# Kernel tuning notes

Measured on AMD Instinct MI355X. Metric: run time of the kernel, lower is better.

The kernel has to match this reference:

```python
import jax, jax.numpy as jnp
import numpy as np


def setup_inputs() -> dict:
    key = jax.random.key(0)
    k1, k2, k3 = jax.random.split(key, 3)
    B, Lq, Lk, D = 8, 512, 512, 64
    q = jax.random.normal(k1, (B, Lq, D), dtype=jnp.float32)
    k = jax.random.normal(k2, (B, Lk, D), dtype=jnp.float32)
    v = jax.random.normal(k3, (B, Lk, D), dtype=jnp.float32)
    return {"q": q, "k": k, "v": v}


def reference(q, k, v):
    scale = 1.0
    # broadcast add: [B, Lq, 1, D] + [B, 1, Lk, D] -> [B, Lq, Lk, D]
    scores = jnp.sum(scale * jnp.tanh(q[:, :, None, :] + k[:, None, :, :]), axis=-1)  # [B, Lq, Lk]
    attn = jax.nn.softmax(scores, axis=-1)
    out = jnp.einsum('bqk,bkd->bqd', attn, v)
    return out
```

## Files before the change

### kernel.cpp

```cpp
#include <hip/hip_runtime.h>

namespace {
constexpr int Bn = 8, LQ = 512, LK = 512, Dn = 64;
constexpr int T = 512, QT = 8, KT = 64, NT = LK / KT;
constexpr float C2 = 2.8853900817779268f;

__device__ __forceinline__ void gload_lds16(const float* g, float* l) {
  __builtin_amdgcn_global_load_lds(
      (const __attribute__((address_space(1))) void*)g,
      (__attribute__((address_space(3))) void*)l, 16, 0, 0);
}

__global__ __launch_bounds__(T, 4)
void addattn(const float* __restrict__ Q, const float* __restrict__ K,
             const float* __restrict__ V, float* __restrict__ O)
{
  __shared__ __align__(16) float ekL[2][KT][68];
  __shared__ __align__(16) float vL [2][KT][Dn];
  __shared__ __align__(16) float eqs[QT][Dn];
  __shared__ __align__(16) float pL [QT][68];
  __shared__ float lsum[QT];

  const int t    = threadIdx.x;
  const int w    = t >> 6;
  const int lane = t & 63;
  const int ks   = (t >> 4) & 3;
  const int dq   = t & 15;
  const int krow = t >> 3;
  const int kc8  = (t & 7) * 8;
  const int bb   = blockIdx.x >> 6;
  const int q0   = (blockIdx.x & 63) * QT;

  const float* Kt = K + (size_t)bb * LK * Dn;
  const float* Vt = V + (size_t)bb * LK * Dn;

  if (t < 128) {
    const int r = t >> 4, d4 = t & 15;
    float4 qv = *(const float4*)(Q + (size_t)(bb * LQ + q0 + r) * Dn + d4 * 4);
    float4 e;
    e.x = __builtin_amdgcn_exp2f(qv.x * C2);
    e.y = __builtin_amdgcn_exp2f(qv.y * C2);
    e.z = __builtin_amdgcn_exp2f(qv.z * C2);
    e.w = __builtin_amdgcn_exp2f(qv.w * C2);
    *(float4*)&eqs[r][d4 * 4] = e;
  }
  {
    const float* g = Vt + (size_t)(w * 8) * Dn + lane * 4;
    float* l = &vL[0][w * 8][0];
    gload_lds16(g, l);
    gload_lds16(g + 256, l + 256);
  }
  {
    float4 k0v = *(const float4*)(Kt + (size_t)krow * Dn + kc8);
    float4 k1v = *(const float4*)(Kt + (size_t)krow * Dn + kc8 + 4);
    float4 e0, e1;
    e0.x = __builtin_amdgcn_exp2f(k0v.x * C2);
    e0.y = __builtin_amdgcn_exp2f(k0v.y * C2);
    e0.z = __builtin_amdgcn_exp2f(k0v.z * C2);
    e0.w = __builtin_amdgcn_exp2f(k0v.w * C2);
    e1.x = __builtin_amdgcn_exp2f(k1v.x * C2);
    e1.y = __builtin_amdgcn_exp2f(k1v.y * C2);
    e1.z = __builtin_amdgcn_exp2f(k1v.z * C2);
    e1.w = __builtin_amdgcn_exp2f(k1v.w * C2);
    *(float4*)&ekL[0][krow][kc8]     = e0;
    *(float4*)&ekL[0][krow][kc8 + 4] = e1;
  }
  __syncthreads();

  float  dsum = 0.f;
  float4 acc  = make_float4(0.f, 0.f, 0.f, 0.f);
  int buf = 0;

  for (int tile = 0; tile < NT; ++tile) {
    float4 kv0, kv1;
    const bool more = (tile + 1 < NT);
    if (more) {
      const int kb = (tile + 1) * KT;
      const float* g = Vt + (size_t)(kb + w * 8) * Dn + lane * 4;
      float* l = &vL[buf ^ 1][w * 8][0];
      gload_lds16(g, l);
      gload_lds16(g + 256, l + 256);
      kv0 = *(const float4*)(Kt + (size_t)(kb + krow) * Dn + kc8);
      kv1 = *(const float4*)(Kt + (size_t)(kb + krow) * Dn + kc8 + 4);
    }

    {
      float a0 = 0.f, a1 = 0.f, a2 = 0.f, a3 = 0.f;
      const float* ekr = &ekL[buf][lane][0];
      const float* eqr = &eqs[w][0];
      #pragma unroll
      for (int d4 = 0; d4 < 16; ++d4) {
        const float4 e = *(const float4*)(eqr + d4 * 4);
        const float4 x = *(const float4*)(ekr + d4 * 4);
        a0 += __builtin_amdgcn_rcpf(fmaf(e.x, x.x, 1.f));
        a1 += __builtin_amdgcn_rcpf(fmaf(e.y, x.y, 1.f));
        a2 += __builtin_amdgcn_rcpf(fmaf(e.z, x.z, 1.f));
        a3 += __builtin_amdgcn_rcpf(fmaf(e.w, x.w, 1.f));
      }
      const float p = __builtin_amdgcn_exp2f(-C2 * ((a0 + a1) + (a2 + a3)));
      dsum += p;
      pL[w][lane] = p;
    }

    {
      const float* vrow = &vL[buf][ks * 16][dq * 4];
      const float* prow = &pL[w][ks * 16];
      #pragma unroll
      for (int j = 0; j < 16; ++j) {
        const float4 v4 = *(const float4*)(vrow + j * Dn);
        const float  pw = prow[j];
        acc.x = fmaf(pw, v4.x, acc.x);
        acc.y = fmaf(pw, v4.y, acc.y);
        acc.z = fmaf(pw, v4.z, acc.z);
        acc.w = fmaf(pw, v4.w, acc.w);
      }
    }

    if (more) {
      float4 e0, e1;
      e0.x = __builtin_amdgcn_exp2f(kv0.x * C2);
      e0.y = __builtin_amdgcn_exp2f(kv0.y * C2);
      e0.z = __builtin_amdgcn_exp2f(kv0.z * C2);
      e0.w = __builtin_amdgcn_exp2f(kv0.w * C2);
      e1.x = __builtin_amdgcn_exp2f(kv1.x * C2);
      e1.y = __builtin_amdgcn_exp2f(kv1.y * C2);
      e1.z = __builtin_amdgcn_exp2f(kv1.z * C2);
      e1.w = __builtin_amdgcn_exp2f(kv1.w * C2);
      *(float4*)&ekL[buf ^ 1][krow][kc8]     = e0;
      *(float4*)&ekL[buf ^ 1][krow][kc8 + 4] = e1;
    }

    __syncthreads();
    buf ^= 1;
  }

  #pragma unroll
  for (int m = 1; m < 64; m <<= 1) dsum += __shfl_xor(dsum, m);
  if (lane == 0) lsum[w] = dsum;

  float* scr = &ekL[0][0][0];
  *(float4*)(scr + (size_t)(w * 4 + ks) * 64 + dq * 4) = acc;
  __syncthreads();

  if (t < 128) {
    const int r = t >> 4, d4 = t & 15;
    float4 o = make_float4(0.f, 0.f, 0.f, 0.f);
    #pragma unroll
    for (int s = 0; s < 4; ++s) {
      const float4 c = *(const float4*)(scr + (size_t)(r * 4 + s) * 64 + d4 * 4);
      o.x += c.x; o.y += c.y; o.z += c.z; o.w += c.w;
    }
    const float inv = 1.0f / lsum[r];
    o.x *= inv; o.y *= inv; o.z *= inv; o.w *= inv;
    *(float4*)(O + (size_t)(bb * LQ + q0 + r) * Dn + d4 * 4) = o;
  }
}
}

extern "C" void kernel_launch(void* const* d_in, const int* in_sizes, int n_in,
                              void* d_out, int out_size, void* d_ws, size_t ws_size,
                              hipStream_t stream) {
  (void)in_sizes; (void)n_in; (void)d_ws; (void)ws_size; (void)out_size;
  const float* Q = (const float*)d_in[0];
  const float* K = (const float*)d_in[1];
  const float* V = (const float*)d_in[2];
  float* O = (float*)d_out;
  addattn<<<dim3(Bn * (LQ / QT)), dim3(T), 0, stream>>>(Q, K, V, O);
}
```

Baseline: 80.99 us.

## Precompute exp(q),exp(k) in prep kernel and register-tile 4 queries per wave

Adds a prep kernel that computes exp2(2x*log2e) for Q and K once into workspace, storing K with an XOR swizzle so LDS reads avoid bank conflicts without padding. The main kernel loads pre-exponentiated K and V tiles straight into LDS via global_load_lds, raises the tile sizes (16 queries, 128 keys), and gives each wave 4 query rows, so every ek and V value loaded is reused four times in registers. This removes the per-block redundant exp of K and cuts LDS traffic per FLOP. In exchange it adds a second launch, workspace traffic, more registers per thread, and half as many blocks.

Result: slower. 92.48 us (+14.2%).

```diff
diff --git a/kernel.cpp b/kernel.cpp
--- a/kernel.cpp
+++ b/kernel.cpp
@@ -2,157 +2,166 @@
 
 namespace {
 constexpr int Bn = 8, LQ = 512, LK = 512, Dn = 64;
-constexpr int T = 512, QT = 8, KT = 64, NT = LK / KT;
+constexpr int T = 512, QT = 16, KT = 128, NT = LK / KT;
 constexpr float C2 = 2.8853900817779268f;
 
-__device__ __forceinline__ void gload_lds16(const float* g, float* l) {
+
+__device__ __forceinline__ void gl_lds16(const float* g, float* l) {
   __builtin_amdgcn_global_load_lds(
       (const __attribute__((address_space(1))) void*)g,
       (__attribute__((address_space(3))) void*)l, 16, 0, 0);
 }
 
-__global__ __launch_bounds__(T, 4)
-void addattn(const float* __restrict__ Q, const float* __restrict__ K,
+__global__ __launch_bounds__(256)
+void prep(const float* __restrict__ Q, const float* __restrict__ K,
+          float* __restrict__ eqG, float* __restrict__ ekG) {
+  const int g = blockIdx.x * 256 + threadIdx.x;
+  const int row = g >> 6, c = g & 63;
+  eqG[g] = __builtin_amdgcn_exp2f(Q[g] * C2);
+  ekG[row * 64 + (c ^ ((row & 7) * 4))] = __builtin_amdgcn_exp2f(K[g] * C2);
+}
+
+__global__ __launch_bounds__(T, 2)
+void addattn(const float* __restrict__ eqG, const float* __restrict__ ekG,
              const float* __restrict__ V, float* __restrict__ O)
 {
-  __shared__ __align__(16) float ekL[2][KT][68];
+  __shared__ __align__(16) float ekL[2][KT][Dn];
   __shared__ __align__(16) float vL [2][KT][Dn];
-  __shared__ __align__(16) float eqs[QT][Dn];
-  __shared__ __align__(16) float pL [QT][68];
-  __shared__ float lsum[QT];
+  __shared__ __align__(16) float pL [QT][132];
+  __shared__ float scrD[8][4];
 
   const int t    = threadIdx.x;
+  const int bb   = blockIdx.x >> 5;
+  const int q0   = (blockIdx.x & 31) * QT;
   const int w    = t >> 6;
   const int lane = t & 63;
-  const int ks   = (t >> 4) & 3;
-  const int dq   = t & 15;
-  const int krow = t >> 3;
-  const int kc8  = (t & 7) * 8;
-  const int bb   = blockIdx.x >> 6;
-  const int q0   = (blockIdx.x & 63) * QT;
+  const int qhu  = __builtin_amdgcn_readfirstlane(w >> 1);
+  const int khu  = __builtin_amdgcn_readfirstlane(w & 1);
+  const int dq   = lane & 15;
+  const int kg   = lane >> 4;
+  const int sw   = (lane & 7) * 4;
 
-  const float* Kt = K + (size_t)bb * LK * Dn;
-  const float* Vt = V + (size_t)bb * LK * Dn;
+  const float* eqw = eqG + (size_t)(bb * LQ + q0 + qhu * 4) * Dn;
+  const float* ekB = ekG + (size_t)(bb * LK) * Dn;
+  const float* vB  = V   + (size_t)(bb * LK) * Dn;
 
-  if (t < 128) {
-    const int r = t >> 4, d4 = t & 15;
-    float4 qv = *(const float4*)(Q + (size_t)(bb * LQ + q0 + r) * Dn + d4 * 4);
-    float4 e;
-    e.x = __builtin_amdgcn_exp2f(qv.x * C2);
-    e.y = __builtin_amdgcn_exp2f(qv.y * C2);
-    e.z = __builtin_amdgcn_exp2f(qv.z * C2);
-    e.w = __builtin_amdgcn_exp2f(qv.w * C2);
-    *(float4*)&eqs[r][d4 * 4] = e;
-  }
-  {
-    const float* g = Vt + (size_t)(w * 8) * Dn + lane * 4;
-    float* l = &vL[0][w * 8][0];
-    gload_lds16(g, l);
-    gload_lds16(g + 256, l + 256);
-  }
-  {
-    float4 k0v = *(const float4*)(Kt + (size_t)krow * Dn + kc8);
-    float4 k1v = *(const float4*)(Kt + (size_t)krow * Dn + kc8 + 4);
-    float4 e0, e1;
-    e0.x = __builtin_amdgcn_exp2f(k0v.x * C2);
-    e0.y = __builtin_amdgcn_exp2f(k0v.y * C2);
-    e0.z = __builtin_amdgcn_exp2f(k0v.z * C2);
-    e0.w = __builtin_amdgcn_exp2f(k0v.w * C2);
-    e1.x = __builtin_amdgcn_exp2f(k1v.x * C2);
-    e1.y = __builtin_amdgcn_exp2f(k1v.y * C2);
-    e1.z = __builtin_amdgcn_exp2f(k1v.z * C2);
-    e1.w = __builtin_amdgcn_exp2f(k1v.w * C2);
-    *(float4*)&ekL[0][krow][kc8]     = e0;
-    *(float4*)&ekL[0][krow][kc8 + 4] = e1;
-  }
+  auto stage = [&](int buf, int k0) {
+    const float* gs = ekB + (size_t)k0 * Dn;
+    const float* vs = vB  + (size_t)k0 * Dn;
+    float* le = &ekL[buf][0][0];
+    float* lv = &vL [buf][0][0];
+    #pragma unroll
+    for (int r = 0; r < 4; ++r) {
+      gl_lds16(gs + r * 2048 + t * 4, le + r * 2048 + t * 4);
+      gl_lds16(vs + r * 2048 + t * 4, lv + r * 2048 + t * 4);
+    }
+  };
+
+  stage(0, 0);
   __syncthreads();
 
-  float  dsum = 0.f;
-  float4 acc  = make_float4(0.f, 0.f, 0.f, 0.f);
-  int buf = 0;
+  float acc[4][4];
+  #pragma unroll
+  for (int qi = 0; qi < 4; ++qi) {
+    acc[qi][0] = 0.f; acc[qi][1] = 0.f; acc[qi][2] = 0.f; acc[qi][3] = 0.f;
+  }
+  float ds4[4] = {0.f, 0.f, 0.f, 0.f};
 
   for (int tile = 0; tile < NT; ++tile) {
-    float4 kv0, kv1;
-    const bool more = (tile + 1 < NT);
-    if (more) {
-      const int kb = (tile + 1) * KT;
-      const float* g = Vt + (size_t)(kb + w * 8) * Dn + lane * 4;
-      float* l = &vL[buf ^ 1][w * 8][0];
-      gload_lds16(g, l);
-      gload_lds16(g + 256, l + 256);
-      kv0 = *(const float4*)(Kt + (size_t)(kb + krow) * Dn + kc8);
-      kv1 = *(const float4*)(Kt + (size_t)(kb + krow) * Dn + kc8 + 4);
-    }
+    const int buf = tile & 1;
+    if (tile + 1 < NT) stage(buf ^ 1, (tile + 1) * KT);
 
     {
-      float a0 = 0.f, a1 = 0.f, a2 = 0.f, a3 = 0.f;
-      const float* ekr = &ekL[buf][lane][0];
-      const float* eqr = &eqs[w][0];
+      const float* ekrow = &ekL[buf][khu * 64 + lane][0];
+      float a0[4] = {0.f, 0.f, 0.f, 0.f};
+      float a1[4] = {0.f, 0.f, 0.f, 0.f};
       #pragma unroll
       for (int d4 = 0; d4 < 16; ++d4) {
-        const float4 e = *(const float4*)(eqr + d4 * 4);
-        const float4 x = *(const float4*)(ekr + d4 * 4);
-        a0 += __builtin_amdgcn_rcpf(fmaf(e.x, x.x, 1.f));
-        a1 += __builtin_amdgcn_rcpf(fmaf(e.y, x.y, 1.f));
-        a2 += __builtin_amdgcn_rcpf(fmaf(e.z, x.z, 1.f));
-        a3 += __builtin_amdgcn_rcpf(fmaf(e.w, x.w, 1.f));
+        const float4 x  = *(const float4*)(ekrow + ((d4 * 4) ^ sw));
+        const float4 e0 = *(const float4*)(eqw + 0 * Dn + d4 * 4);
+        const float4 e1 = *(const float4*)(eqw + 1 * Dn + d4 * 4);
+        const float4 e2 = *(const float4*)(eqw + 2 * Dn + d4 * 4);
+        const float4 e3 = *(const float4*)(eqw + 3 * Dn + d4 * 4);
+        a0[0] += __builtin_amdgcn_rcpf(fmaf(e0.x, x.x, 1.f));
+        a1[0] += __builtin_amdgcn_rcpf(fmaf(e0.y, x.y, 1.f));
+        a0[0] += __builtin_amdgcn_rcpf(fmaf(e0.z, x.z, 1.f));
+        a1[0] += __builtin_amdgcn_rcpf(fmaf(e0.w, x.w, 1.f));
+        a0[1] += __builtin_amdgcn_rcpf(fmaf(e1.x, x.x, 1.f));
+        a1[1] += __builtin_amdgcn_rcpf(fmaf(e1.y, x.y, 1.f));
+        a0[1] += __builtin_amdgcn_rcpf(fmaf(e1.z, x.z, 1.f));
+        a1[1] += __builtin_amdgcn_rcpf(fmaf(e1.w, x.w, 1.f));
+        a0[2] += __builtin_amdgcn_rcpf(fmaf(e2.x, x.x, 1.f));
+        a1[2] += __builtin_amdgcn_rcpf(fmaf(e2.y, x.y, 1.f));
+        a0[2] += __builtin_amdgcn_rcpf(fmaf(e2.z, x.z, 1.f));
+        a1[2] += __builtin_amdgcn_rcpf(fmaf(e2.w, x.w, 1.f));
+        a0[3] += __builtin_amdgcn_rcpf(fmaf(e3.x, x.x, 1.f));
+        a1[3] += __builtin_amdgcn_rcpf(fmaf(e3.y, x.y, 1.f));
+        a0[3] += __builtin_amdgcn_rcpf(fmaf(e3.z, x.z, 1.f));
+        a1[3] += __builtin_amdgcn_rcpf(fmaf(e3.w, x.w, 1.f));
       }
-      const float p = __builtin_amdgcn_exp2f(-C2 * ((a0 + a1) + (a2 + a3)));
-      dsum += p;
-      pL[w][lane] = p;
-    }
-
-    {
-      const float* vrow = &vL[buf][ks * 16][dq * 4];
-      const float* prow = &pL[w][ks * 16];
       #pragma unroll
-      for (int j = 0; j < 16; ++j) {
-        const float4 v4 = *(const float4*)(vrow + j * Dn);
-        const float  pw = prow[j];
-        acc.x = fmaf(pw, v4.x, acc.x);
-        acc.y = fmaf(pw, v4.y, acc.y);
-        acc.z = fmaf(pw, v4.z, acc.z);
-        acc.w = fmaf(pw, v4.w, acc.w);
+      for (int qi = 0; qi < 4; ++qi) {
+        const float p = __builtin_amdgcn_exp2f(-C2 * (a0[qi] + a1[qi]));
+        ds4[qi] += p;
+        pL[qhu * 4 + qi][khu * 64 + lane] = p;
       }
     }
 
-    if (more) {
-      float4 e0, e1;
-      e0.x = __builtin_amdgcn_exp2f(kv0.x * C2);
-      e0.y = __builtin_amdgcn_exp2f(kv0.y * C2);
-      e0.z = __builtin_amdgcn_exp2f(kv0.z * C2);
-      e0.w = __builtin_amdgcn_exp2f(kv0.w * C2);
-      e1.x = __builtin_amdgcn_exp2f(kv1.x * C2);
-      e1.y = __builtin_amdgcn_exp2f(kv1.y * C2);
-      e1.z = __builtin_amdgcn_exp2f(kv1.z * C2);
-      e1.w = __builtin_amdgcn_exp2f(kv1.w * C2);
-      *(float4*)&ekL[buf ^ 1][krow][kc8]     = e0;
-      *(float4*)&ekL[buf ^ 1][krow][kc8 + 4] = e1;
+    float pcf[4][16];
+    #pragma unroll
+    for (int qi = 0; qi < 4; ++qi)
+      #pragma unroll
+      for (int jq = 0; jq < 4; ++jq)
+        *(float4*)&pcf[qi][jq * 4] =
+            *(const float4*)&pL[qhu * 4 + qi][khu * 64 + kg * 16 + jq * 4];
+
+    {
+      const float* vbase = &vL[buf][khu * 64 + kg * 16][0] + dq * 4;
+      #pragma unroll
+      for (int j = 0; j < 16; ++j) {
+        const float4 v4 = *(const float4*)(vbase + j * Dn);
+        #pragma unroll
+        for (int qi = 0; qi < 4; ++qi) {
+          const float pj = pcf[qi][j];
+          acc[qi][0] = fmaf(pj, v4.x, acc[qi][0]);
+          acc[qi][1] = fmaf(pj, v4.y, acc[qi][1]);
+          acc[qi][2] = fmaf(pj, v4.z, acc[qi][2]);
+          acc[qi][3] = fmaf(pj, v4.w, acc[qi][3]);
+        }
+      }
     }
 
     __syncthreads();
-    buf ^= 1;
   }
 
   #pragma unroll
-  for (int m = 1; m < 64; m <<= 1) dsum += __shfl_xor(dsum, m);
-  if (lane == 0) lsum[w] = dsum;
+  for (int qi = 0; qi < 4; ++qi) {
+    float s = ds4[qi];
+    #pragma unroll
+    for (int m = 1; m < 64; m <<= 1) s += __shfl_xor(s, m);
+    if (lane == 0) scrD[w][qi] = s;
+  }
 
   float* scr = &ekL[0][0][0];
-  *(float4*)(scr + (size_t)(w * 4 + ks) * 64 + dq * 4) = acc;
+  const int slice = khu * 4 + kg;
+  #pragma unroll
+  for (int qi = 0; qi < 4; ++qi)
+    *(float4*)(scr + (size_t)(slice * QT + qhu * 4 + qi) * Dn + dq * 4) =
+        make_float4(acc[qi][0], acc[qi][1], acc[qi][2], acc[qi][3]);
   __syncthreads();
 
-  if (t < 128) {
-    const int r = t >> 4, d4 = t & 15;
+  if (t < 256) {
+    const int r = t >> 4, d4c = t & 15;
     float4 o = make_float4(0.f, 0.f, 0.f, 0.f);
     #pragma unroll
-    for (int s = 0; s < 4; ++s) {
-      const float4 c = *(const float4*)(scr + (size_t)(r * 4 + s) * 64 + d4 * 4);
+    for (int s8 = 0; s8 < 8; ++s8) {
+      const float4 c = *(const float4*)(scr + (size_t)(s8 * QT + r) * Dn + d4c * 4);
       o.x += c.x; o.y += c.y; o.z += c.z; o.w += c.w;
     }
-    const float inv = 1.0f / lsum[r];
+    const int rqh = r >> 2, rqi = r & 3;
+    const float inv = 1.0f / (scrD[rqh * 2 + 0][rqi] + scrD[rqh * 2 + 1][rqi]);
     o.x *= inv; o.y *= inv; o.z *= inv; o.w *= inv;
-    *(float4*)(O + (size_t)(bb * LQ + q0 + r) * Dn + d4 * 4) = o;
+    *(float4*)(O + (size_t)(bb * LQ + q0 + r) * Dn + d4c * 4) = o;
   }
 }
 }
@@ -160,10 +169,13 @@
 extern "C" void kernel_launch(void* const* d_in, const int* in_sizes, int n_in,
                               void* d_out, int out_size, void* d_ws, size_t ws_size,
                               hipStream_t stream) {
-  (void)in_sizes; (void)n_in; (void)d_ws; (void)ws_size; (void)out_size;
+  (void)in_sizes; (void)n_in; (void)out_size; (void)ws_size;
   const float* Q = (const float*)d_in[0];
   const float* K = (const float*)d_in[1];
   const float* V = (const float*)d_in[2];
-  float* O = (float*)d_out;
-  addattn<<<dim3(Bn * (LQ / QT)), dim3(T), 0, stream>>>(Q, K, V, O);
+  float* O   = (float*)d_out;
+  float* eqG = (float*)d_ws;
+  float* ekG = eqG + (size_t)Bn * LQ * Dn;
+  prep<<<dim3(Bn * LK * Dn / 256), dim3(256), 0, stream>>>(Q, K, eqG, ekG);
+  addattn<<<dim3(Bn * (LQ / QT)), dim3(T), 0, stream>>>(eqG, ekG, V, O);
 }
```

## Register-tile exp(q) per wave, split D across lanes with shuffle reduction

Applied to the files above, without the earlier changes.

Each wave now handles two query rows and half of the key tile. Four lanes share one key column and each covers 16 of the D dimensions, reducing partial sums with shuffles. exp(q) values stay in registers instead of shared memory, and each exp(k) LDS load is reused for two queries, which halves LDS traffic in the score loop. The P·V stage and the final reduction are remapped to match. This adds register pressure and extra shuffles.

Result: slower. 83.39 us (+3.0%).

```diff
diff --git a/kernel.cpp b/kernel.cpp
--- a/kernel.cpp
+++ b/kernel.cpp
@@ -5,7 +5,8 @@
 constexpr int T = 512, QT = 8, KT = 64, NT = LK / KT;
 constexpr float C2 = 2.8853900817779268f;
 
-__device__ __forceinline__ void gload_lds16(const float* g, float* l) {
+
+__device__ __forceinline__ void gl_lds16(const float* g, float* l) {
   __builtin_amdgcn_global_load_lds(
       (const __attribute__((address_space(1))) void*)g,
       (__attribute__((address_space(3))) void*)l, 16, 0, 0);
@@ -17,98 +18,151 @@
 {
   __shared__ __align__(16) float ekL[2][KT][68];
   __shared__ __align__(16) float vL [2][KT][Dn];
-  __shared__ __align__(16) float eqs[QT][Dn];
   __shared__ __align__(16) float pL [QT][68];
-  __shared__ float lsum[QT];
+  __shared__ float scrD[2][QT];
 
   const int t    = threadIdx.x;
   const int w    = t >> 6;
   const int lane = t & 63;
-  const int ks   = (t >> 4) & 3;
-  const int dq   = t & 15;
-  const int krow = t >> 3;
-  const int kc8  = (t & 7) * 8;
+  const int qq   = w >> 1;
+  const int kq   = w & 1;
+  const int dsub = lane & 3;
+  const int k16  = lane >> 2;
+  const int pq   = lane >> 5;
+  const int kh   = (lane >> 4) & 1;
+  const int dq   = lane & 15;
+  const int srow = t >> 3;
+  const int scol = (t & 7) * 8;
   const int bb   = blockIdx.x >> 6;
   const int q0   = (blockIdx.x & 63) * QT;
 
   const float* Kt = K + (size_t)bb * LK * Dn;
   const float* Vt = V + (size_t)bb * LK * Dn;
 
-  if (t < 128) {
-    const int r = t >> 4, d4 = t & 15;
-    float4 qv = *(const float4*)(Q + (size_t)(bb * LQ + q0 + r) * Dn + d4 * 4);
-    float4 e;
-    e.x = __builtin_amdgcn_exp2f(qv.x * C2);
-    e.y = __builtin_amdgcn_exp2f(qv.y * C2);
-    e.z = __builtin_amdgcn_exp2f(qv.z * C2);
-    e.w = __builtin_amdgcn_exp2f(qv.w * C2);
-    *(float4*)&eqs[r][d4 * 4] = e;
-  }
+  auto stageV = [&](int buf, int k0) {
+    const float* vs = Vt + (size_t)k0 * Dn;
+    float* lv = &vL[buf][0][0];
+    gl_lds16(vs + t * 4,        lv + t * 4);
+    gl_lds16(vs + 2048 + t * 4, lv + 2048 + t * 4);
+  };
+
+  float4 eqr[8];
+  #pragma unroll
+  for (int q = 0; q < 2; ++q) {
+    #pragma unroll
+    for (int j = 0; j < 4; ++j) {
+      float4 v = *(const float4*)(Q + (size_t)(bb * LQ + q0 + qq * 2 + q) * Dn
+                                  + dsub * 16 + j * 4);
+      v.x = __builtin_amdgcn_exp2f(v.x * C2);
+      v.y = __builtin_amdgcn_exp2f(v.y * C2);
+      v.z = __builtin_amdgcn_exp2f(v.z * C2);
+      v.w = __builtin_amdgcn_exp2f(v.w * C2);
+      eqr[q * 4 + j] = v;
+    }
+  }
+
+  stageV(0, 0);
   {
-    const float* g = Vt + (size_t)(w * 8) * Dn + lane * 4;
-    float* l = &vL[0][w * 8][0];
-    gload_lds16(g, l);
-    gload_lds16(g + 256, l + 256);
-  }
-  {
-    float4 k0v = *(const float4*)(Kt + (size_t)krow * Dn + kc8);
-    float4 k1v = *(const float4*)(Kt + (size_t)krow * Dn + kc8 + 4);
-    float4 e0, e1;
-    e0.x = __builtin_amdgcn_exp2f(k0v.x * C2);
-    e0.y = __builtin_amdgcn_exp2f(k0v.y * C2);
-    e0.z = __builtin_amdgcn_exp2f(k0v.z * C2);
-    e0.w = __builtin_amdgcn_exp2f(k0v.w * C2);
-    e1.x = __builtin_amdgcn_exp2f(k1v.x * C2);
-    e1.y = __builtin_amdgcn_exp2f(k1v.y * C2);
-    e1.z = __builtin_amdgcn_exp2f(k1v.z * C2);
-    e1.w = __builtin_amdgcn_exp2f(k1v.w * C2);
-    *(float4*)&ekL[0][krow][kc8]     = e0;
-    *(float4*)&ekL[0][krow][kc8 + 4] = e1;
+    const float* kx = Kt + (size_t)srow * Dn + scol;
+    float4 ka = *(const float4*)kx;
+    float4 kb = *(const float4*)(kx + 4);
+    float4 ea, eb;
+    ea.x = __builtin_amdgcn_exp2f(ka.x * C2);
+    ea.y = __builtin_amdgcn_exp2f(ka.y * C2);
+    ea.z = __builtin_amdgcn_exp2f(ka.z * C2);
+    ea.w = __builtin_amdgcn_exp2f(ka.w * C2);
+    eb.x = __builtin_amdgcn_exp2f(kb.x * C2);
+    eb.y = __builtin_amdgcn_exp2f(kb.y * C2);
+    eb.z = __builtin_amdgcn_exp2f(kb.z * C2);
+    eb.w = __builtin_amdgcn_exp2f(kb.w * C2);
+    *(float4*)&ekL[0][srow][scol]     = ea;
+    *(float4*)&ekL[0][srow][scol + 4] = eb;
   }
   __syncthreads();
 
-  float  dsum = 0.f;
-  float4 acc  = make_float4(0.f, 0.f, 0.f, 0.f);
-  int buf = 0;
+  float dsum0 = 0.f, dsum1 = 0.f;
+  float4 acc = make_float4(0.f, 0.f, 0.f, 0.f);
 
   for (int tile = 0; tile < NT; ++tile) {
-    float4 kv0, kv1;
+    const int buf = tile & 1;
     const bool more = (tile + 1 < NT);
+    float4 nk0, nk1;
     if (more) {
       const int kb = (tile + 1) * KT;
-      const float* g = Vt + (size_t)(kb + w * 8) * Dn + lane * 4;
-      float* l = &vL[buf ^ 1][w * 8][0];
-      gload_lds16(g, l);
-      gload_lds16(g + 256, l + 256);
-      kv0 = *(const float4*)(Kt + (size_t)(kb + krow) * Dn + kc8);
-      kv1 = *(const float4*)(Kt + (size_t)(kb + krow) * Dn + kc8 + 4);
+      stageV(buf ^ 1, kb);
+      const float* kx = Kt + (size_t)(kb + srow) * Dn + scol;
+      nk0 = *(const float4*)kx;
+      nk1 = *(const float4*)(kx + 4);
+    }
+
+    #pragma unroll
+    for (int ki = 0; ki < 2; ++ki) {
+      const int kcol = kq * 32 + ki * 16 + k16;
+      const float* ekr = &ekL[buf][kcol][dsub * 16];
+      const float4 x0 = *(const float4*)(ekr);
+      const float4 x1 = *(const float4*)(ekr + 4);
+      const float4 x2 = *(const float4*)(ekr + 8);
+      const float4 x3 = *(const float4*)(ekr + 12);
+      float a0 = 0.f, b0 = 0.f, a1 = 0.f, b1 = 0.f;
+      {
+        const float4 e0 = eqr[0], e1 = eqr[1], e2 = eqr[2], e3 = eqr[3];
+        a0 += __builtin_amdgcn_rcpf(fmaf(e0.x, x0.x, 1.f));
+        a0 += __builtin_amdgcn_rcpf(fmaf(e0.y, x0.y, 1.f));
+        a0 += __builtin_amdgcn_rcpf(fmaf(e0.z, x0.z, 1.f));
+        a0 += __builtin_amdgcn_rcpf(fmaf(e0.w, x0.w, 1.f));
+        a0 += __builtin_amdgcn_rcpf(fmaf(e1.x, x1.x, 1.f));
+        a0 += __builtin_amdgcn_rcpf(fmaf(e1.y, x1.y, 1.f));
+        a0 += __builtin_amdgcn_rcpf(fmaf(e1.z, x1.z, 1.f));
+        a0 += __builtin_amdgcn_rcpf(fmaf(e1.w, x1.w, 1.f));
+        b0 += __builtin_amdgcn_rcpf(fmaf(e2.x, x2.x, 1.f));
+        b0 += __builtin_amdgcn_rcpf(fmaf(e2.y, x2.y, 1.f));
+        b0 += __builtin_amdgcn_rcpf(fmaf(e2.z, x2.z, 1.f));
+        b0 += __builtin_amdgcn_rcpf(fmaf(e2.w, x2.w, 1.f));
+        b0 += __builtin_amdgcn_rcpf(fmaf(e3.x, x3.x, 1.f));
+        b0 += __builtin_amdgcn_rcpf(fmaf(e3.y, x3.y, 1.f));
+        b0 += __builtin_amdgcn_rcpf(fmaf(e3.z, x3.z, 1.f));
+        b0 += __builtin_amdgcn_rcpf(fmaf(e3.w, x3.w, 1.f));
+      }
+      {
+        const float4 e0 = eqr[4], e1 = eqr[5], e2 = eqr[6], e3 = eqr[7];
+        a1 += __builtin_amdgcn_rcpf(fmaf(e0.x, x0.x, 1.f));
+        a1 += __builtin_amdgcn_rcpf(fmaf(e0.y, x0.y, 1.f));
+        a1 += __builtin_amdgcn_rcpf(fmaf(e0.z, x0.z, 1.f));
+        a1 += __builtin_amdgcn_rcpf(fmaf(e0.w, x0.w, 1.f));
+        a1 += __builtin_amdgcn_rcpf(fmaf(e1.x, x1.x, 1.f));
+        a1 += __builtin_amdgcn_rcpf(fmaf(e1.y, x1.y, 1.f));
+        a1 += __builtin_amdgcn_rcpf(fmaf(e1.z, x1.z, 1.f));
+        a1 += __builtin_amdgcn_rcpf(fmaf(e1.w, x1.w, 1.f));
+        b1 += __builtin_amdgcn_rcpf(fmaf(e2.x, x2.x, 1.f));
+        b1 += __builtin_amdgcn_rcpf(fmaf(e2.y, x2.y, 1.f));
+        b1 += __builtin_amdgcn_rcpf(fmaf(e2.z, x2.z, 1.f));
+        b1 += __builtin_amdgcn_rcpf(fmaf(e2.w, x2.w, 1.f));
+        b1 += __builtin_amdgcn_rcpf(fmaf(e3.x, x3.x, 1.f));
+        b1 += __builtin_amdgcn_rcpf(fmaf(e3.y, x3.y, 1.f));
+        b1 += __builtin_amdgcn_rcpf(fmaf(e3.z, x3.z, 1.f));
+        b1 += __builtin_amdgcn_rcpf(fmaf(e3.w, x3.w, 1.f));
+      }
+      float s0 = a0 + b0, s1 = a1 + b1;
+      s0 += __shfl_xor(s0, 1);  s0 += __shfl_xor(s0, 2);
+      s1 += __shfl_xor(s1, 1);  s1 += __shfl_xor(s1, 2);
+      const float p0 = __builtin_amdgcn_exp2f(-C2 * s0);
+      const float p1 = __builtin_amdgcn_exp2f(-C2 * s1);
+      dsum0 += p0;
+      dsum1 += p1;
+      if (dsub < 2) pL[qq * 2 + dsub][kcol] = dsub ? p1 : p0;
     }
 
     {
-      float a0 = 0.f, a1 = 0.f, a2 = 0.f, a3 = 0.f;
-      const float* ekr = &ekL[buf][lane][0];
-      const float* eqr = &eqs[w][0];
+      const float* pr = &pL[qq * 2 + pq][kq * 32 + kh * 16];
+      float pcf[16];
       #pragma unroll
-      for (int d4 = 0; d4 < 16; ++d4) {
-        const float4 e = *(const float4*)(eqr + d4 * 4);
-        const float4 x = *(const float4*)(ekr + d4 * 4);
-        a0 += __builtin_amdgcn_rcpf(fmaf(e.x, x.x, 1.f));
-        a1 += __builtin_amdgcn_rcpf(fmaf(e.y, x.y, 1.f));
-        a2 += __builtin_amdgcn_rcpf(fmaf(e.z, x.z, 1.f));
-        a3 += __builtin_amdgcn_rcpf(fmaf(e.w, x.w, 1.f));
-      }
-      const float p = __builtin_amdgcn_exp2f(-C2 * ((a0 + a1) + (a2 + a3)));
-      dsum += p;
-      pL[w][lane] = p;
-    }
-
-    {
-      const float* vrow = &vL[buf][ks * 16][dq * 4];
-      const float* prow = &pL[w][ks * 16];
+      for (int j4 = 0; j4 < 4; ++j4)
+        *(float4*)&pcf[j4 * 4] = *(const float4*)(pr + j4 * 4);
+      const float* vb = &vL[buf][kq * 32 + kh * 16][dq * 4];
       #pragma unroll
       for (int j = 0; j < 16; ++j) {
-        const float4 v4 = *(const float4*)(vrow + j * Dn);
-        const float  pw = prow[j];
+        const float4 v4 = *(const float4*)(vb + j * Dn);
+        const float  pw = pcf[j];
         acc.x = fmaf(pw, v4.x, acc.x);
         acc.y = fmaf(pw, v4.y, acc.y);
         acc.z = fmaf(pw, v4.z, acc.z);
@@ -117,29 +171,35 @@
     }
 
     if (more) {
-      float4 e0, e1;
-      e0.x = __builtin_amdgcn_exp2f(kv0.x * C2);
-      e0.y = __builtin_amdgcn_exp2f(kv0.y * C2);
-      e0.z = __builtin_amdgcn_exp2f(kv0.z * C2);
-      e0.w = __builtin_amdgcn_exp2f(kv0.w * C2);
-      e1.x = __builtin_amdgcn_exp2f(kv1.x * C2);
-      e1.y = __builtin_amdgcn_exp2f(kv1.y * C2);
-      e1.z = __builtin_amdgcn_exp2f(kv1.z * C2);
-      e1.w = __builtin_amdgcn_exp2f(kv1.w * C2);
-      *(float4*)&ekL[buf ^ 1][krow][kc8]     = e0;
-      *(float4*)&ekL[buf ^ 1][krow][kc8 + 4] = e1;
+      float4 ea, eb;
+      ea.x = __builtin_amdgcn_exp2f(nk0.x * C2);
+      ea.y = __builtin_amdgcn_exp2f(nk0.y * C2);
+      ea.z = __builtin_amdgcn_exp2f(nk0.z * C2);
+      ea.w = __builtin_amdgcn_exp2f(nk0.w * C2);
+      eb.x = __builtin_amdgcn_exp2f(nk1.x * C2);
+      eb.y = __builtin_amdgcn_exp2f(nk1.y * C2);
+      eb.z = __builtin_amdgcn_exp2f(nk1.z * C2);
+      eb.w = __builtin_amdgcn_exp2f(nk1.w * C2);
+      *(float4*)&ekL[buf ^ 1][srow][scol]     = ea;
+      *(float4*)&ekL[buf ^ 1][srow][scol + 4] = eb;
     }
 
     __syncthreads();
-    buf ^= 1;
-  }
-
+  }
+
+  float s0 = dsum0, s1 = dsum1;
   #pragma unroll
-  for (int m = 1; m < 64; m <<= 1) dsum += __shfl_xor(dsum, m);
-  if (lane == 0) lsum[w] = dsum;
-
-  float* scr = &ekL[0][0][0];
-  *(float4*)(scr + (size_t)(w * 4 + ks) * 64 + dq * 4) = acc;
+  for (int m = 4; m < 64; m <<= 1) {
+    s0 += __shfl_xor(s0, m);
+    s1 += __shfl_xor(s1, m);
+  }
+  if (lane == 0) {
+    scrD[kq][qq * 2 + 0] = s0;
+    scrD[kq][qq * 2 + 1] = s1;
+  }
+
+  float* scrO = &ekL[0][0][0];
+  *(float4*)(scrO + (size_t)(((kq * 2 + kh) * 8) + qq * 2 + pq) * 64 + dq * 4) = acc;
   __syncthreads();
 
   if (t < 128) {
@@ -147,10 +207,10 @@
     float4 o = make_float4(0.f, 0.f, 0.f, 0.f);
     #pragma unroll
     for (int s = 0; s < 4; ++s) {
-      const float4 c = *(const float4*)(scr + (size_t)(r * 4 + s) * 64 + d4 * 4);
+      const float4 c = *(const float4*)(scrO + (size_t)(s * 8 + r) * 64 + d4 * 4);
       o.x += c.x; o.y += c.y; o.z += c.z; o.w += c.w;
     }
-    const float inv = 1.0f / lsum[r];
+    const float inv = 1.0f / (scrD[0][r] + scrD[1][r]);
     o.x *= inv; o.y *= inv; o.z *= inv; o.w *= inv;
     *(float4*)(O + (size_t)(bb * LQ + q0 + r) * Dn + d4 * 4) = o;
   }
```
